# Kernel optimization log

Measured on AMD Instinct MI355X. Metric: run time of the kernel, lower is better.

The kernel has to match this reference:

```python
import jax, jax.numpy as jnp
import numpy as np

N_NODES = 100000
N_HEDGES = 25000
NNZ = 1600000
IN_CH = 128
HEADS_OUT = 128  # heads * out_channels = 8 * 16


def setup_inputs() -> dict:
    key = jax.random.key(0)
    k1, k2, k3, k4, k5, k6 = jax.random.split(key, 6)
    X = jax.random.normal(k1, (N_NODES, IN_CH), dtype=jnp.float32)
    Wlin = jax.random.normal(k2, (IN_CH, HEADS_OUT), dtype=jnp.float32) * (1.0 / np.sqrt(IN_CH))
    degE = jax.random.uniform(k3, (N_HEDGES, 1), dtype=jnp.float32)
    degV = jax.random.uniform(k4, (N_NODES, 1), dtype=jnp.float32)
    W = jnp.ones((N_HEDGES, 1), dtype=jnp.float32)
    g1_src = jax.random.randint(k5, (NNZ,), 0, N_NODES, dtype=jnp.int32)
    g1_dst = jax.random.randint(k6, (NNZ,), 0, N_HEDGES, dtype=jnp.int32)
    return {"X": X, "Wlin": Wlin, "degE": degE, "degV": degV, "W": W,
            "g1_src": g1_src, "g1_dst": g1_dst}


def reference(X, Wlin, degE, degV, W, g1_src, g1_dst):
    # Linear projection (no bias): [N, in_ch] @ [in_ch, heads*out] -> [N, HO]
    Xp = X @ Wlin
    # Stage 1: copy_u_sum over g1 (node -> hyperedge): out[e] = sum_{v in e} Xp[v]
    Xe = jax.ops.segment_sum(Xp[g1_src], g1_dst, num_segments=N_HEDGES)
    # Elementwise hyperedge scaling: degE then W (W is ones buffer in original)
    Xe = Xe * degE * W
    # Stage 2: copy_u_sum over g2 = g1^T (hyperedge -> node)
    Xv = jax.ops.segment_sum(Xe[g1_dst], g1_src, num_segments=N_NODES)
    # Node degree scaling
    Xv = Xv * degV
    return Xv
```

## Files before the change

### kernel.cpp

```cpp
#include <hip/hip_runtime.h>
#include <hip/hip_bf16.h>


#define CAPE 128
#define CAPV 64

typedef __attribute__((ext_vector_type(8))) short bf16x8;
typedef __attribute__((ext_vector_type(4))) float f32x4;
typedef __attribute__((ext_vector_type(8))) float f32x8;

__device__ __forceinline__ unsigned short f32_to_bf16(float f) {
    unsigned int u = __float_as_uint(f);
    u += 0x7FFFu + ((u >> 16) & 1u);
    return (unsigned short)(u >> 16);
}
__device__ __forceinline__ float bf16_to_f32(unsigned short h) {
    return __uint_as_float(((unsigned int)h) << 16);
}

__global__ __launch_bounds__(256) void wt_bf16(const float* __restrict__ Wl,
                                               unsigned short* __restrict__ Wt) {
    int idx = blockIdx.x * 256 + threadIdx.x;
    if (idx < 128 * 128) {
        int n = idx >> 7, k = idx & 127;
        Wt[idx] = f32_to_bf16(Wl[k * 128 + n]);
    }
}

__global__ __launch_bounds__(256) void zero_i(int* __restrict__ p, int n) {
    int i = blockIdx.x * 256 + threadIdx.x;
    if (i < n) p[i] = 0;
}

#define LDK 136
__global__ __launch_bounds__(256) void k2_fillE_gemm(const int* __restrict__ src,
                                                     const int* __restrict__ dst,
                                                     int* __restrict__ cntE,
                                                     int* __restrict__ adjE,
                                                     int nnz, int nFill,
                                                     const float* __restrict__ X,
                                                     const unsigned short* __restrict__ Wt,
                                                     unsigned short* __restrict__ Xp,
                                                     int nrows, int nGemm) {
    __shared__ unsigned short XsB[64 * LDK];
    __shared__ unsigned short WtB[128 * LDK];

    const int role = blockIdx.x & 1;
    const int id   = blockIdx.x >> 1;
    const int tid  = threadIdx.x;

    if (role == 0) {
        if (id >= nFill) return;
        const int base = id * 1024 + tid;
        int s[4], d[4], p[4];
        bool ok[4];
#pragma unroll
        for (int j = 0; j < 4; ++j) {
            int e = base + j * 256;
            ok[j] = (e < nnz);
            s[j] = ok[j] ? src[e] : 0;
            d[j] = ok[j] ? dst[e] : 0;
        }
#pragma unroll
        for (int j = 0; j < 4; ++j)
            if (ok[j]) p[j] = atomicAdd(&cntE[d[j]], 1);
#pragma unroll
        for (int j = 0; j < 4; ++j)
            if (ok[j] && p[j] < CAPE) adjE[(long)d[j] * CAPE + p[j]] = s[j];
        return;
    }

    if (id >= nGemm) return;
    const int row0 = id * 64;

    for (int base = tid * 4; base < 64 * 128; base += 1024) {
        int r = base >> 7, c = base & 127;
        float4 v = make_float4(0.f, 0.f, 0.f, 0.f);
        if (row0 + r < nrows) v = *(const float4*)(X + (long)(row0 + r) * 128 + c);
        ushort4 h;
        h.x = f32_to_bf16(v.x); h.y = f32_to_bf16(v.y);
        h.z = f32_to_bf16(v.z); h.w = f32_to_bf16(v.w);
        *(ushort4*)(XsB + r * LDK + c) = h;
    }
    for (int base = tid * 4; base < 128 * 128; base += 1024) {
        int n = base >> 7, k = base & 127;
        ushort4 h = *(const ushort4*)(Wt + base);
        *(ushort4*)(WtB + n * LDK + k) = h;
    }
    __syncthreads();

    const int w    = tid >> 6;
    const int lane = tid & 63;
    const int m    = lane & 15;
    const int quad = lane >> 4;

    f32x4 acc[8];
#pragma unroll
    for (int ct = 0; ct < 8; ++ct) acc[ct] = (f32x4){0.f, 0.f, 0.f, 0.f};

#pragma unroll
    for (int kk = 0; kk < 4; ++kk) {
        bf16x8 a = *(const bf16x8*)(XsB + (w * 16 + m) * LDK + kk * 32 + quad * 8);
#pragma unroll
        for (int ct = 0; ct < 8; ++ct) {
            bf16x8 b = *(const bf16x8*)(WtB + (ct * 16 + m) * LDK + kk * 32 + quad * 8);
            acc[ct] = __builtin_amdgcn_mfma_f32_16x16x32_bf16(a, b, acc[ct], 0, 0, 0);
        }
    }

#pragma unroll
    for (int ct = 0; ct < 8; ++ct) {
#pragma unroll
        for (int r = 0; r < 4; ++r) {
            int row = row0 + w * 16 + quad * 4 + r;
            if (row < nrows)
                Xp[(long)row * 128 + ct * 16 + m] = f32_to_bf16(acc[ct][r]);
        }
    }
}

__global__ __launch_bounds__(256) void k3_fillV_gatherE(const int* __restrict__ src,
                                                        const int* __restrict__ dst,
                                                        int* __restrict__ cntV,
                                                        unsigned short* __restrict__ adjV,
                                                        int nnz, int nFill,
                                                        const unsigned short* __restrict__ Xp,
                                                        const int* __restrict__ cntE,
                                                        const int* __restrict__ adjE,
                                                        const float* __restrict__ degE,
                                                        const float* __restrict__ Wbuf,
                                                        unsigned short* __restrict__ Xe,
                                                        int nE, int nGath) {
    const int role = blockIdx.x & 1;
    const int id   = blockIdx.x >> 1;
    const int tid  = threadIdx.x;

    if (role == 0) {
        if (id >= nFill) return;
        const int base = id * 1024 + tid;
        int s[4], d[4], p[4];
        bool ok[4];
#pragma unroll
        for (int j = 0; j < 4; ++j) {
            int e = base + j * 256;
            ok[j] = (e < nnz);
            s[j] = ok[j] ? src[e] : 0;
            d[j] = ok[j] ? dst[e] : 0;
        }
#pragma unroll
        for (int j = 0; j < 4; ++j)
            if (ok[j]) p[j] = atomicAdd(&cntV[s[j]], 1);
#pragma unroll
        for (int j = 0; j < 4; ++j)
            if (ok[j] && p[j] < CAPV) adjV[(long)s[j] * CAPV + p[j]] = (unsigned short)d[j];
        return;
    }

    if (id >= nGath) return;
    int t = id * 256 + tid;
    int e = t >> 4;
    if (e >= nE) return;
    int c = (t & 15) << 3;
    int len = cntE[e];
    if (len > CAPE) len = CAPE;
    const int* adj = adjE + (long)e * CAPE;
    float acc[8];
#pragma unroll
    for (int q = 0; q < 8; ++q) acc[q] = 0.f;

    int i = 0;
    for (; i + 8 <= len; i += 8) {
        int4 a0 = *(const int4*)(adj + i);
        int4 a1 = *(const int4*)(adj + i + 4);
        int v[8] = {a0.x, a0.y, a0.z, a0.w, a1.x, a1.y, a1.z, a1.w};
        bf16x8 h[8];
#pragma unroll
        for (int j = 0; j < 8; ++j)
            h[j] = *(const bf16x8*)(Xp + (long)v[j] * 128 + c);
#pragma unroll
        for (int j = 0; j < 8; ++j)
#pragma unroll
            for (int q = 0; q < 8; ++q)
                acc[q] += bf16_to_f32((unsigned short)h[j][q]);
    }
    for (; i + 4 <= len; i += 4) {
        int4 a0 = *(const int4*)(adj + i);
        int v[4] = {a0.x, a0.y, a0.z, a0.w};
        bf16x8 h[4];
#pragma unroll
        for (int j = 0; j < 4; ++j)
            h[j] = *(const bf16x8*)(Xp + (long)v[j] * 128 + c);
#pragma unroll
        for (int j = 0; j < 4; ++j)
#pragma unroll
            for (int q = 0; q < 8; ++q)
                acc[q] += bf16_to_f32((unsigned short)h[j][q]);
    }
    for (; i < len; ++i) {
        int v = adj[i];
        bf16x8 h = *(const bf16x8*)(Xp + (long)v * 128 + c);
#pragma unroll
        for (int q = 0; q < 8; ++q)
            acc[q] += bf16_to_f32((unsigned short)h[q]);
    }

    float sc = degE[e] * Wbuf[e];
    bf16x8 o;
#pragma unroll
    for (int q = 0; q < 8; ++q) o[q] = (short)f32_to_bf16(acc[q] * sc);
    *(bf16x8*)(Xe + (long)e * 128 + c) = o;
}

__global__ __launch_bounds__(256) void gather_nodes_b(const unsigned short* __restrict__ Xe,
                                                      const int* __restrict__ cntV,
                                                      const unsigned short* __restrict__ adjV,
                                                      const float* __restrict__ degV,
                                                      float* __restrict__ out,
                                                      int nV) {
    int t = blockIdx.x * 256 + threadIdx.x;
    int v = t >> 4;
    if (v >= nV) return;
    int c = (t & 15) << 3;
    int len = cntV[v];
    if (len > CAPV) len = CAPV;
    const unsigned short* adj = adjV + (long)v * CAPV;
    float acc[8];
#pragma unroll
    for (int q = 0; q < 8; ++q) acc[q] = 0.f;

    int i = 0;
    for (; i + 8 <= len; i += 8) {
        ushort4 a0 = *(const ushort4*)(adj + i);
        ushort4 a1 = *(const ushort4*)(adj + i + 4);
        int e[8] = {a0.x, a0.y, a0.z, a0.w, a1.x, a1.y, a1.z, a1.w};
        bf16x8 h[8];
#pragma unroll
        for (int j = 0; j < 8; ++j)
            h[j] = *(const bf16x8*)(Xe + (long)e[j] * 128 + c);
#pragma unroll
        for (int j = 0; j < 8; ++j)
#pragma unroll
            for (int q = 0; q < 8; ++q)
                acc[q] += bf16_to_f32((unsigned short)h[j][q]);
    }
    for (; i + 4 <= len; i += 4) {
        ushort4 a0 = *(const ushort4*)(adj + i);
        int e[4] = {a0.x, a0.y, a0.z, a0.w};
        bf16x8 h[4];
#pragma unroll
        for (int j = 0; j < 4; ++j)
            h[j] = *(const bf16x8*)(Xe + (long)e[j] * 128 + c);
#pragma unroll
        for (int j = 0; j < 4; ++j)
#pragma unroll
            for (int q = 0; q < 8; ++q)
                acc[q] += bf16_to_f32((unsigned short)h[j][q]);
    }
    for (; i < len; ++i) {
        int e = adj[i];
        bf16x8 h = *(const bf16x8*)(Xe + (long)e * 128 + c);
#pragma unroll
        for (int q = 0; q < 8; ++q)
            acc[q] += bf16_to_f32((unsigned short)h[q]);
    }

    float sc = degV[v];
    f32x8 o;
#pragma unroll
    for (int q = 0; q < 8; ++q) o[q] = acc[q] * sc;
    *(f32x8*)(out + (long)v * 128 + c) = o;
}

__global__ __launch_bounds__(256) void zero_f4(float4* __restrict__ p, int n4) {
    int i = blockIdx.x * 256 + threadIdx.x;
    if (i < n4) p[i] = make_float4(0.f, 0.f, 0.f, 0.f);
}

__global__ __launch_bounds__(256) void gemm_xw_f32(const float* __restrict__ X,
                                                   const float* __restrict__ Wl,
                                                   float* __restrict__ Xp,
                                                   int nrows) {
    __shared__ float Xs[32 * 128];
    const int tid = threadIdx.x;
    const int row0 = blockIdx.x * 32;
    for (int i = tid * 4; i < 32 * 128; i += 256 * 4) {
        int r = row0 + (i >> 7);
        float4 v = make_float4(0.f, 0.f, 0.f, 0.f);
        if (r < nrows) v = *(const float4*)(X + (long)row0 * 128 + i);
        *(float4*)(Xs + i) = v;
    }
    __syncthreads();
    const int col = tid & 127;
    const int rg  = (tid >> 7) * 16;
    float acc[16];
#pragma unroll
    for (int r = 0; r < 16; ++r) acc[r] = 0.f;
    for (int k = 0; k < 128; k += 4) {
        const float w0 = Wl[(k + 0) * 128 + col];
        const float w1 = Wl[(k + 1) * 128 + col];
        const float w2 = Wl[(k + 2) * 128 + col];
        const float w3 = Wl[(k + 3) * 128 + col];
#pragma unroll
        for (int r = 0; r < 16; ++r) {
            float4 x = *(const float4*)(Xs + (rg + r) * 128 + k);
            acc[r] = fmaf(x.w, w3, fmaf(x.z, w2, fmaf(x.y, w1, fmaf(x.x, w0, acc[r]))));
        }
    }
#pragma unroll
    for (int r = 0; r < 16; ++r) {
        int row = row0 + rg + r;
        if (row < nrows) Xp[(long)row * 128 + col] = acc[r];
    }
}

__global__ __launch_bounds__(256) void scatter_to_hedges(const float* __restrict__ Xp,
                                                         const int* __restrict__ src,
                                                         const int* __restrict__ dst,
                                                         float* __restrict__ Xe,
                                                         int nnz) {
    int t = blockIdx.x * 256 + threadIdx.x;
    int e = t >> 5;
    if (e >= nnz) return;
    int c = (t & 31) << 2;
    int s = src[e], d = dst[e];
    float4 v = *(const float4*)(Xp + (long)s * 128 + c);
    float* o = Xe + (long)d * 128 + c;
    atomicAdd(o + 0, v.x); atomicAdd(o + 1, v.y);
    atomicAdd(o + 2, v.z); atomicAdd(o + 3, v.w);
}

__global__ __launch_bounds__(256) void scatter_to_nodes(const float* __restrict__ Xe,
                                                        const int* __restrict__ src,
                                                        const int* __restrict__ dst,
                                                        const float* __restrict__ degE,
                                                        const float* __restrict__ Wbuf,
                                                        const float* __restrict__ degV,
                                                        float* __restrict__ out,
                                                        int nnz) {
    int t = blockIdx.x * 256 + threadIdx.x;
    int e = t >> 5;
    if (e >= nnz) return;
    int c = (t & 31) << 2;
    int s = src[e], d = dst[e];
    float sc = degE[d] * Wbuf[d] * degV[s];
    float4 v = *(const float4*)(Xe + (long)d * 128 + c);
    float* o = out + (long)s * 128 + c;
    atomicAdd(o + 0, v.x * sc); atomicAdd(o + 1, v.y * sc);
    atomicAdd(o + 2, v.z * sc); atomicAdd(o + 3, v.w * sc);
}

extern "C" void kernel_launch(void* const* d_in, const int* in_sizes, int n_in,
                              void* d_out, int out_size, void* d_ws, size_t ws_size,
                              hipStream_t stream) {
    const float* X    = (const float*)d_in[0];
    const float* Wlin = (const float*)d_in[1];
    const float* degE = (const float*)d_in[2];
    const float* degV = (const float*)d_in[3];
    const float* Wbuf = (const float*)d_in[4];
    const int* g1_src = (const int*)d_in[5];
    const int* g1_dst = (const int*)d_in[6];

    const int nE  = in_sizes[2];
    const int nV  = in_sizes[3];
    const int nnz = in_sizes[5];

    float* out = (float*)d_out;
    char* ws = (char*)d_ws;

    size_t boff = 0;
    unsigned short* Xe = (unsigned short*)(ws + boff); boff += (size_t)nE * 128 * 2;
    int* cntE   = (int*)(ws + boff);              boff += (size_t)nE * 4;
    int* cntV   = (int*)(ws + boff);              boff += (size_t)nV * 4;
    int* adjE   = (int*)(ws + boff);              boff += (size_t)nE * CAPE * 4;
    unsigned short* adjV = (unsigned short*)(ws + boff); boff += (size_t)nV * CAPV * 2;
    unsigned short* Wt   = (unsigned short*)(ws + boff); boff += (size_t)128 * 128 * 2;

    if (boff <= ws_size) {
        unsigned short* Xp_bf = (unsigned short*)d_out;

        wt_bf16<<<64, 256, 0, stream>>>(Wlin, Wt);

        int ncnt = nE + nV;
        zero_i<<<(ncnt + 255) / 256, 256, 0, stream>>>(cntE, ncnt);

        int nFill = (nnz + 1023) / 1024;
        int nGemm = (nV + 63) / 64;
        int k2max = (nFill > nGemm) ? nFill : nGemm;
        k2_fillE_gemm<<<2 * k2max, 256, 0, stream>>>(g1_src, g1_dst, cntE, adjE, nnz, nFill,
                                                     X, Wt, Xp_bf, nV, nGemm);

        int nGath = (nE * 16 + 255) / 256;
        int nGrp  = (nFill > nGath) ? nFill : nGath;
        k3_fillV_gatherE<<<2 * nGrp, 256, 0, stream>>>(g1_src, g1_dst, cntV, adjV, nnz, nFill,
                                                       Xp_bf, cntE, adjE, degE, Wbuf, Xe,
                                                       nE, nGath);

        long t = (long)nV * 16;
        gather_nodes_b<<<(int)((t + 255) / 256), 256, 0, stream>>>(Xe, cntV, adjV,
                                                                   degV, out, nV);
    } else {
        float* XeF = (float*)d_ws;
        float* Xp  = out;
        int n4 = nE * 128 / 4;
        zero_f4<<<(n4 + 255) / 256, 256, 0, stream>>>((float4*)XeF, n4);
        gemm_xw_f32<<<(nV + 31) / 32, 256, 0, stream>>>(X, Wlin, Xp, nV);
        long th = (long)nnz * 32;
        scatter_to_hedges<<<(int)((th + 255) / 256), 256, 0, stream>>>(Xp, g1_src, g1_dst,
                                                                       XeF, nnz);
        int m4 = out_size / 4;
        zero_f4<<<(m4 + 255) / 256, 256, 0, stream>>>((float4*)out, m4);
        scatter_to_nodes<<<(int)((th + 255) / 256), 256, 0, stream>>>(XeF, g1_src, g1_dst,
                                                                      degE, Wbuf, degV,
                                                                      out, nnz);
    }
}
```

Measured before the change: 335.4 us.

## Split adjacency fills and gathers into ranged chunks co-scheduled across kernels

Builds the hyperedge and node adjacency lists in key-range chunks: hyperedges in two halves, nodes in three thirds. Each fill chunk is paired in one launch with a gather over a range whose adjacency is already complete, so atomic-heavy list building overlaps bandwidth-bound gathering. The node gather no longer waits for the whole node fill to finish. The weight transpose and counter zeroing are also merged into one init kernel. In exchange, the src/dst index arrays are rescanned on every fill pass, and there are more kernel launches in total.

```diff
diff --git a/kernel.cpp b/kernel.cpp
--- a/kernel.cpp
+++ b/kernel.cpp
@@ -18,30 +18,205 @@
     return __uint_as_float(((unsigned int)h) << 16);
 }
 
-__global__ __launch_bounds__(256) void wt_bf16(const float* __restrict__ Wl,
-                                               unsigned short* __restrict__ Wt) {
-    int idx = blockIdx.x * 256 + threadIdx.x;
-    if (idx < 128 * 128) {
+
+__device__ __forceinline__ void fillE_body(const int* __restrict__ src,
+                                           const int* __restrict__ dst,
+                                           int* __restrict__ cntE,
+                                           int* __restrict__ adjE,
+                                           int nnz, int id, int tid,
+                                           int lo, int hi) {
+    const int base = id * 1024 + tid;
+    int s[4], d[4], p[4];
+    bool ok[4];
+#pragma unroll
+    for (int j = 0; j < 4; ++j) {
+        int e = base + j * 256;
+        bool in = (e < nnz);
+        s[j] = in ? src[e] : 0;
+        d[j] = in ? dst[e] : lo - 1;
+        ok[j] = in && d[j] >= lo && d[j] < hi;
+    }
+#pragma unroll
+    for (int j = 0; j < 4; ++j)
+        if (ok[j]) p[j] = atomicAdd(&cntE[d[j]], 1);
+#pragma unroll
+    for (int j = 0; j < 4; ++j)
+        if (ok[j] && p[j] < CAPE) adjE[(long)d[j] * CAPE + p[j]] = s[j];
+}
+
+__device__ __forceinline__ void fillV_body(const int* __restrict__ src,
+                                           const int* __restrict__ dst,
+                                           int* __restrict__ cntV,
+                                           unsigned short* __restrict__ adjV,
+                                           int nnz, int id, int tid,
+                                           int lo, int hi) {
+    const int base = id * 1024 + tid;
+    int s[4], d[4], p[4];
+    bool ok[4];
+#pragma unroll
+    for (int j = 0; j < 4; ++j) {
+        int e = base + j * 256;
+        bool in = (e < nnz);
+        s[j] = in ? src[e] : lo - 1;
+        d[j] = in ? dst[e] : 0;
+        ok[j] = in && s[j] >= lo && s[j] < hi;
+    }
+#pragma unroll
+    for (int j = 0; j < 4; ++j)
+        if (ok[j]) p[j] = atomicAdd(&cntV[s[j]], 1);
+#pragma unroll
+    for (int j = 0; j < 4; ++j)
+        if (ok[j] && p[j] < CAPV) adjV[(long)s[j] * CAPV + p[j]] = (unsigned short)d[j];
+}
+
+__device__ __forceinline__ void gatherE_body(int id, int tid,
+                                             const unsigned short* __restrict__ Xp,
+                                             const int* __restrict__ cntE,
+                                             const int* __restrict__ adjE,
+                                             const float* __restrict__ degE,
+                                             const float* __restrict__ Wbuf,
+                                             unsigned short* __restrict__ Xe,
+                                             int eLo, int eHi) {
+    int t = id * 256 + tid;
+    int e = eLo + (t >> 4);
+    if (e >= eHi) return;
+    int c = (t & 15) << 3;
+    int len = cntE[e];
+    if (len > CAPE) len = CAPE;
+    const int* adj = adjE + (long)e * CAPE;
+    float acc[8];
+#pragma unroll
+    for (int q = 0; q < 8; ++q) acc[q] = 0.f;
+
+    int i = 0;
+    for (; i + 8 <= len; i += 8) {
+        int4 a0 = *(const int4*)(adj + i);
+        int4 a1 = *(const int4*)(adj + i + 4);
+        int v[8] = {a0.x, a0.y, a0.z, a0.w, a1.x, a1.y, a1.z, a1.w};
+        bf16x8 h[8];
+#pragma unroll
+        for (int j = 0; j < 8; ++j)
+            h[j] = *(const bf16x8*)(Xp + (long)v[j] * 128 + c);
+#pragma unroll
+        for (int j = 0; j < 8; ++j)
+#pragma unroll
+            for (int q = 0; q < 8; ++q)
+                acc[q] += bf16_to_f32((unsigned short)h[j][q]);
+    }
+    for (; i + 4 <= len; i += 4) {
+        int4 a0 = *(const int4*)(adj + i);
+        int v[4] = {a0.x, a0.y, a0.z, a0.w};
+        bf16x8 h[4];
+#pragma unroll
+        for (int j = 0; j < 4; ++j)
+            h[j] = *(const bf16x8*)(Xp + (long)v[j] * 128 + c);
+#pragma unroll
+        for (int j = 0; j < 4; ++j)
+#pragma unroll
+            for (int q = 0; q < 8; ++q)
+                acc[q] += bf16_to_f32((unsigned short)h[j][q]);
+    }
+    for (; i < len; ++i) {
+        int v = adj[i];
+        bf16x8 h = *(const bf16x8*)(Xp + (long)v * 128 + c);
+#pragma unroll
+        for (int q = 0; q < 8; ++q)
+            acc[q] += bf16_to_f32((unsigned short)h[q]);
+    }
+
+    float sc = degE[e] * Wbuf[e];
+    bf16x8 o;
+#pragma unroll
+    for (int q = 0; q < 8; ++q) o[q] = (short)f32_to_bf16(acc[q] * sc);
+    *(bf16x8*)(Xe + (long)e * 128 + c) = o;
+}
+
+__device__ __forceinline__ void gatherV_body(int id, int tid,
+                                             const unsigned short* __restrict__ Xe,
+                                             const int* __restrict__ cntV,
+                                             const unsigned short* __restrict__ adjV,
+                                             const float* __restrict__ degV,
+                                             float* __restrict__ out,
+                                             int vLo, int vHi) {
+    int t = id * 256 + tid;
+    int v = vLo + (t >> 4);
+    if (v >= vHi) return;
+    int c = (t & 15) << 3;
+    int len = cntV[v];
+    if (len > CAPV) len = CAPV;
+    const unsigned short* adj = adjV + (long)v * CAPV;
+    float acc[8];
+#pragma unroll
+    for (int q = 0; q < 8; ++q) acc[q] = 0.f;
+
+    int i = 0;
+    for (; i + 8 <= len; i += 8) {
+        ushort4 a0 = *(const ushort4*)(adj + i);
+        ushort4 a1 = *(const ushort4*)(adj + i + 4);
+        int e[8] = {a0.x, a0.y, a0.z, a0.w, a1.x, a1.y, a1.z, a1.w};
+        bf16x8 h[8];
+#pragma unroll
+        for (int j = 0; j < 8; ++j)
+            h[j] = *(const bf16x8*)(Xe + (long)e[j] * 128 + c);
+#pragma unroll
+        for (int j = 0; j < 8; ++j)
+#pragma unroll
+            for (int q = 0; q < 8; ++q)
+                acc[q] += bf16_to_f32((unsigned short)h[j][q]);
+    }
+    for (; i + 4 <= len; i += 4) {
+        ushort4 a0 = *(const ushort4*)(adj + i);
+        int e[4] = {a0.x, a0.y, a0.z, a0.w};
+        bf16x8 h[4];
+#pragma unroll
+        for (int j = 0; j < 4; ++j)
+            h[j] = *(const bf16x8*)(Xe + (long)e[j] * 128 + c);
+#pragma unroll
+        for (int j = 0; j < 4; ++j)
+#pragma unroll
+            for (int q = 0; q < 8; ++q)
+                acc[q] += bf16_to_f32((unsigned short)h[j][q]);
+    }
+    for (; i < len; ++i) {
+        int e = adj[i];
+        bf16x8 h = *(const bf16x8*)(Xe + (long)e * 128 + c);
+#pragma unroll
+        for (int q = 0; q < 8; ++q)
+            acc[q] += bf16_to_f32((unsigned short)h[q]);
+    }
+
+    float sc = degV[v];
+    f32x8 o;
+#pragma unroll
+    for (int q = 0; q < 8; ++q) o[q] = acc[q] * sc;
+    *(f32x8*)(out + (long)v * 128 + c) = o;
+}
+
+
+__global__ __launch_bounds__(256) void k_init(const float* __restrict__ Wl,
+                                              unsigned short* __restrict__ Wt,
+                                              int* __restrict__ cnt, int ncnt) {
+    int b = blockIdx.x;
+    if (b < 64) {
+        int idx = b * 256 + threadIdx.x;
         int n = idx >> 7, k = idx & 127;
         Wt[idx] = f32_to_bf16(Wl[k * 128 + n]);
-    }
-}
-
-__global__ __launch_bounds__(256) void zero_i(int* __restrict__ p, int n) {
-    int i = blockIdx.x * 256 + threadIdx.x;
-    if (i < n) p[i] = 0;
+    } else {
+        int i = (b - 64) * 256 + threadIdx.x;
+        if (i < ncnt) cnt[i] = 0;
+    }
 }
 
 #define LDK 136
-__global__ __launch_bounds__(256) void k2_fillE_gemm(const int* __restrict__ src,
-                                                     const int* __restrict__ dst,
-                                                     int* __restrict__ cntE,
-                                                     int* __restrict__ adjE,
-                                                     int nnz, int nFill,
-                                                     const float* __restrict__ X,
-                                                     const unsigned short* __restrict__ Wt,
-                                                     unsigned short* __restrict__ Xp,
-                                                     int nrows, int nGemm) {
+__global__ __launch_bounds__(256) void k_fillE_gemm(const int* __restrict__ src,
+                                                    const int* __restrict__ dst,
+                                                    int* __restrict__ cntE,
+                                                    int* __restrict__ adjE,
+                                                    int nnz, int nFill, int eLo, int eHi,
+                                                    const float* __restrict__ X,
+                                                    const unsigned short* __restrict__ Wt,
+                                                    unsigned short* __restrict__ Xp,
+                                                    int nrows, int nGemm) {
     __shared__ unsigned short XsB[64 * LDK];
     __shared__ unsigned short WtB[128 * LDK];
 
@@ -50,23 +225,7 @@
     const int tid  = threadIdx.x;
 
     if (role == 0) {
-        if (id >= nFill) return;
-        const int base = id * 1024 + tid;
-        int s[4], d[4], p[4];
-        bool ok[4];
-#pragma unroll
-        for (int j = 0; j < 4; ++j) {
-            int e = base + j * 256;
-            ok[j] = (e < nnz);
-            s[j] = ok[j] ? src[e] : 0;
-            d[j] = ok[j] ? dst[e] : 0;
-        }
-#pragma unroll
-        for (int j = 0; j < 4; ++j)
-            if (ok[j]) p[j] = atomicAdd(&cntE[d[j]], 1);
-#pragma unroll
-        for (int j = 0; j < 4; ++j)
-            if (ok[j] && p[j] < CAPE) adjE[(long)d[j] * CAPE + p[j]] = s[j];
+        if (id < nFill) fillE_body(src, dst, cntE, adjE, nnz, id, tid, eLo, eHi);
         return;
     }
 
@@ -119,156 +278,74 @@
     }
 }
 
-__global__ __launch_bounds__(256) void k3_fillV_gatherE(const int* __restrict__ src,
-                                                        const int* __restrict__ dst,
-                                                        int* __restrict__ cntV,
-                                                        unsigned short* __restrict__ adjV,
-                                                        int nnz, int nFill,
-                                                        const unsigned short* __restrict__ Xp,
-                                                        const int* __restrict__ cntE,
-                                                        const int* __restrict__ adjE,
-                                                        const float* __restrict__ degE,
-                                                        const float* __restrict__ Wbuf,
-                                                        unsigned short* __restrict__ Xe,
-                                                        int nE, int nGath) {
+__global__ __launch_bounds__(256) void k_fillE_gatherE(const int* __restrict__ src,
+                                                       const int* __restrict__ dst,
+                                                       int* __restrict__ cntE,
+                                                       int* __restrict__ adjE,
+                                                       int nnz, int nFill, int eLo, int eHi,
+                                                       const unsigned short* __restrict__ Xp,
+                                                       const float* __restrict__ degE,
+                                                       const float* __restrict__ Wbuf,
+                                                       unsigned short* __restrict__ Xe,
+                                                       int geLo, int geHi) {
     const int role = blockIdx.x & 1;
     const int id   = blockIdx.x >> 1;
     const int tid  = threadIdx.x;
-
     if (role == 0) {
-        if (id >= nFill) return;
-        const int base = id * 1024 + tid;
-        int s[4], d[4], p[4];
-        bool ok[4];
-#pragma unroll
-        for (int j = 0; j < 4; ++j) {
-            int e = base + j * 256;
-            ok[j] = (e < nnz);
-            s[j] = ok[j] ? src[e] : 0;
-            d[j] = ok[j] ? dst[e] : 0;
-        }
-#pragma unroll
-        for (int j = 0; j < 4; ++j)
-            if (ok[j]) p[j] = atomicAdd(&cntV[s[j]], 1);
-#pragma unroll
-        for (int j = 0; j < 4; ++j)
-            if (ok[j] && p[j] < CAPV) adjV[(long)s[j] * CAPV + p[j]] = (unsigned short)d[j];
-        return;
-    }
-
-    if (id >= nGath) return;
-    int t = id * 256 + tid;
-    int e = t >> 4;
-    if (e >= nE) return;
-    int c = (t & 15) << 3;
-    int len = cntE[e];
-    if (len > CAPE) len = CAPE;
-    const int* adj = adjE + (long)e * CAPE;
-    float acc[8];
-#pragma unroll
-    for (int q = 0; q < 8; ++q) acc[q] = 0.f;
-
-    int i = 0;
-    for (; i + 8 <= len; i += 8) {
-        int4 a0 = *(const int4*)(adj + i);
-        int4 a1 = *(const int4*)(adj + i + 4);
-        int v[8] = {a0.x, a0.y, a0.z, a0.w, a1.x, a1.y, a1.z, a1.w};
-        bf16x8 h[8];
-#pragma unroll
-        for (int j = 0; j < 8; ++j)
-            h[j] = *(const bf16x8*)(Xp + (long)v[j] * 128 + c);
-#pragma unroll
-        for (int j = 0; j < 8; ++j)
-#pragma unroll
-            for (int q = 0; q < 8; ++q)
-                acc[q] += bf16_to_f32((unsigned short)h[j][q]);
-    }
-    for (; i + 4 <= len; i += 4) {
-        int4 a0 = *(const int4*)(adj + i);
-        int v[4] = {a0.x, a0.y, a0.z, a0.w};
-        bf16x8 h[4];
-#pragma unroll
-        for (int j = 0; j < 4; ++j)
-            h[j] = *(const bf16x8*)(Xp + (long)v[j] * 128 + c);
-#pragma unroll
-        for (int j = 0; j < 4; ++j)
-#pragma unroll
-            for (int q = 0; q < 8; ++q)
-                acc[q] += bf16_to_f32((unsigned short)h[j][q]);
-    }
-    for (; i < len; ++i) {
-        int v = adj[i];
-        bf16x8 h = *(const bf16x8*)(Xp + (long)v * 128 + c);
-#pragma unroll
-        for (int q = 0; q < 8; ++q)
-            acc[q] += bf16_to_f32((unsigned short)h[q]);
-    }
-
-    float sc = degE[e] * Wbuf[e];
-    bf16x8 o;
-#pragma unroll
-    for (int q = 0; q < 8; ++q) o[q] = (short)f32_to_bf16(acc[q] * sc);
-    *(bf16x8*)(Xe + (long)e * 128 + c) = o;
-}
-
-__global__ __launch_bounds__(256) void gather_nodes_b(const unsigned short* __restrict__ Xe,
-                                                      const int* __restrict__ cntV,
-                                                      const unsigned short* __restrict__ adjV,
-                                                      const float* __restrict__ degV,
-                                                      float* __restrict__ out,
-                                                      int nV) {
-    int t = blockIdx.x * 256 + threadIdx.x;
-    int v = t >> 4;
-    if (v >= nV) return;
-    int c = (t & 15) << 3;
-    int len = cntV[v];
-    if (len > CAPV) len = CAPV;
-    const unsigned short* adj = adjV + (long)v * CAPV;
-    float acc[8];
-#pragma unroll
-    for (int q = 0; q < 8; ++q) acc[q] = 0.f;
-
-    int i = 0;
-    for (; i + 8 <= len; i += 8) {
-        ushort4 a0 = *(const ushort4*)(adj + i);
-        ushort4 a1 = *(const ushort4*)(adj + i + 4);
-        int e[8] = {a0.x, a0.y, a0.z, a0.w, a1.x, a1.y, a1.z, a1.w};
-        bf16x8 h[8];
-#pragma unroll
-        for (int j = 0; j < 8; ++j)
-            h[j] = *(const bf16x8*)(Xe + (long)e[j] * 128 + c);
-#pragma unroll
-        for (int j = 0; j < 8; ++j)
-#pragma unroll
-            for (int q = 0; q < 8; ++q)
-                acc[q] += bf16_to_f32((unsigned short)h[j][q]);
-    }
-    for (; i + 4 <= len; i += 4) {
-        ushort4 a0 = *(const ushort4*)(adj + i);
-        int e[4] = {a0.x, a0.y, a0.z, a0.w};
-        bf16x8 h[4];
-#pragma unroll
-        for (int j = 0; j < 4; ++j)
-            h[j] = *(const bf16x8*)(Xe + (long)e[j] * 128 + c);
-#pragma unroll
-        for (int j = 0; j < 4; ++j)
-#pragma unroll
-            for (int q = 0; q < 8; ++q)
-                acc[q] += bf16_to_f32((unsigned short)h[j][q]);
-    }
-    for (; i < len; ++i) {
-        int e = adj[i];
-        bf16x8 h = *(const bf16x8*)(Xe + (long)e * 128 + c);
-#pragma unroll
-        for (int q = 0; q < 8; ++q)
-            acc[q] += bf16_to_f32((unsigned short)h[q]);
-    }
-
-    float sc = degV[v];
-    f32x8 o;
-#pragma unroll
-    for (int q = 0; q < 8; ++q) o[q] = acc[q] * sc;
-    *(f32x8*)(out + (long)v * 128 + c) = o;
+        if (id < nFill) fillE_body(src, dst, cntE, adjE, nnz, id, tid, eLo, eHi);
+    } else {
+        gatherE_body(id, tid, Xp, cntE, adjE, degE, Wbuf, Xe, geLo, geHi);
+    }
+}
+
+__global__ __launch_bounds__(256) void k_fillV_gatherE(const int* __restrict__ src,
+                                                       const int* __restrict__ dst,
+                                                       int* __restrict__ cntV,
+                                                       unsigned short* __restrict__ adjV,
+                                                       int nnz, int nFill, int vLo, int vHi,
+                                                       const unsigned short* __restrict__ Xp,
+                                                       const int* __restrict__ cntE,
+                                                       const int* __restrict__ adjE,
+                                                       const float* __restrict__ degE,
+                                                       const float* __restrict__ Wbuf,
+                                                       unsigned short* __restrict__ Xe,
+                                                       int geLo, int geHi) {
+    const int role = blockIdx.x & 1;
+    const int id   = blockIdx.x >> 1;
+    const int tid  = threadIdx.x;
+    if (role == 0) {
+        if (id < nFill) fillV_body(src, dst, cntV, adjV, nnz, id, tid, vLo, vHi);
+    } else {
+        gatherE_body(id, tid, Xp, cntE, adjE, degE, Wbuf, Xe, geLo, geHi);
+    }
+}
+
+__global__ __launch_bounds__(256) void k_fillV_gatherV(const int* __restrict__ src,
+                                                       const int* __restrict__ dst,
+                                                       int* __restrict__ cntV,
+                                                       unsigned short* __restrict__ adjV,
+                                                       int nnz, int nFill, int vLo, int vHi,
+                                                       const unsigned short* __restrict__ Xe,
+                                                       const float* __restrict__ degV,
+                                                       float* __restrict__ out,
+                                                       int gvLo, int gvHi) {
+    const int role = blockIdx.x & 1;
+    const int id   = blockIdx.x >> 1;
+    const int tid  = threadIdx.x;
+    if (role == 0) {
+        if (id < nFill) fillV_body(src, dst, cntV, adjV, nnz, id, tid, vLo, vHi);
+    } else {
+        gatherV_body(id, tid, Xe, cntV, adjV, degV, out, gvLo, gvHi);
+    }
+}
+
+__global__ __launch_bounds__(256) void k_gatherV(const unsigned short* __restrict__ Xe,
+                                                 const int* __restrict__ cntV,
+                                                 const unsigned short* __restrict__ adjV,
+                                                 const float* __restrict__ degV,
+                                                 float* __restrict__ out,
+                                                 int gvLo, int gvHi) {
+    gatherV_body(blockIdx.x, threadIdx.x, Xe, cntV, adjV, degV, out, gvLo, gvHi);
 }
 
 __global__ __launch_bounds__(256) void zero_f4(float4* __restrict__ p, int n4) {
@@ -378,26 +455,43 @@
     if (boff <= ws_size) {
         unsigned short* Xp_bf = (unsigned short*)d_out;
 
-        wt_bf16<<<64, 256, 0, stream>>>(Wlin, Wt);
+        const int nFill = (nnz + 1023) / 1024;
+        const int nGemm = (nV + 63) / 64;
+        const int eMid  = nE / 2;
+        const int v1 = (nV / 3) & ~15;
+        const int v2 = ((2 * nV) / 3) & ~15;
 
         int ncnt = nE + nV;
-        zero_i<<<(ncnt + 255) / 256, 256, 0, stream>>>(cntE, ncnt);
-
-        int nFill = (nnz + 1023) / 1024;
-        int nGemm = (nV + 63) / 64;
-        int k2max = (nFill > nGemm) ? nFill : nGemm;
-        k2_fillE_gemm<<<2 * k2max, 256, 0, stream>>>(g1_src, g1_dst, cntE, adjE, nnz, nFill,
-                                                     X, Wt, Xp_bf, nV, nGemm);
-
-        int nGath = (nE * 16 + 255) / 256;
-        int nGrp  = (nFill > nGath) ? nFill : nGath;
-        k3_fillV_gatherE<<<2 * nGrp, 256, 0, stream>>>(g1_src, g1_dst, cntV, adjV, nnz, nFill,
-                                                       Xp_bf, cntE, adjE, degE, Wbuf, Xe,
-                                                       nE, nGath);
-
-        long t = (long)nV * 16;
-        gather_nodes_b<<<(int)((t + 255) / 256), 256, 0, stream>>>(Xe, cntV, adjV,
-                                                                   degV, out, nV);
+        k_init<<<64 + (ncnt + 255) / 256, 256, 0, stream>>>(Wlin, Wt, cntE, ncnt);
+
+        int g2a = 2 * ((nFill > nGemm) ? nFill : nGemm);
+        k_fillE_gemm<<<g2a, 256, 0, stream>>>(g1_src, g1_dst, cntE, adjE, nnz, nFill,
+                                              0, eMid, X, Wt, Xp_bf, nV, nGemm);
+
+        int nGE1 = (eMid * 16 + 255) / 256;
+        int g2b = 2 * ((nFill > nGE1) ? nFill : nGE1);
+        k_fillE_gatherE<<<g2b, 256, 0, stream>>>(g1_src, g1_dst, cntE, adjE, nnz, nFill,
+                                                 eMid, nE, Xp_bf, degE, Wbuf, Xe,
+                                                 0, eMid);
+
+        int nGE2 = ((nE - eMid) * 16 + 255) / 256;
+        int g3 = 2 * ((nFill > nGE2) ? nFill : nGE2);
+        k_fillV_gatherE<<<g3, 256, 0, stream>>>(g1_src, g1_dst, cntV, adjV, nnz, nFill,
+                                                0, v1, Xp_bf, cntE, adjE, degE, Wbuf, Xe,
+                                                eMid, nE);
+
+        int nGV1 = (v1 * 16 + 255) / 256;
+        int g4 = 2 * ((nFill > nGV1) ? nFill : nGV1);
+        k_fillV_gatherV<<<g4, 256, 0, stream>>>(g1_src, g1_dst, cntV, adjV, nnz, nFill,
+                                                v1, v2, Xe, degV, out, 0, v1);
+
+        int nGV2 = ((v2 - v1) * 16 + 255) / 256;
+        int g5 = 2 * ((nFill > nGV2) ? nFill : nGV2);
+        k_fillV_gatherV<<<g5, 256, 0, stream>>>(g1_src, g1_dst, cntV, adjV, nnz, nFill,
+                                                v2, nV, Xe, degV, out, v1, v2);
+
+        int nGV3 = ((nV - v2) * 16 + 255) / 256;
+        k_gatherV<<<nGV3, 256, 0, stream>>>(Xe, cntV, adjV, degV, out, v2, nV);
     } else {
         float* XeF = (float*)d_ws;
         float* Xp  = out;
```

Result: slower. 357.0 us (+6.4%).

## Build adjacency lists with chunked LDS histograms and scan instead of global atomics

Applied to the files above, without the earlier changes.

Replaces the global-atomic bucket fill of both adjacency lists with a three-pass build. Each block histograms one chunk of edges into packed 8-bit counters held in shared memory, a scan kernel turns these into per-chunk offsets, and a scatter pass writes the slots using shared-memory atomics. The GEMM and fill roles are split back into separate kernels, and the histV and Xe buffers share one region. The aim is to remove contention from global atomics. The cost is extra passes over src/dst, a byte-per-chunk histogram that can overflow when a chunk holds more than 255 edges for one key, and a serial per-column scan.

```diff
diff --git a/kernel.cpp b/kernel.cpp
--- a/kernel.cpp
+++ b/kernel.cpp
@@ -4,6 +4,8 @@
 
 #define CAPE 128
 #define CAPV 64
+#define LDK  136
+#define RW   6250
 
 typedef __attribute__((ext_vector_type(8))) short bf16x8;
 typedef __attribute__((ext_vector_type(4))) float f32x4;
@@ -18,8 +20,8 @@
     return __uint_as_float(((unsigned int)h) << 16);
 }
 
-__global__ __launch_bounds__(256) void wt_bf16(const float* __restrict__ Wl,
-                                               unsigned short* __restrict__ Wt) {
+__global__ __launch_bounds__(256) void k_init(const float* __restrict__ Wl,
+                                              unsigned short* __restrict__ Wt) {
     int idx = blockIdx.x * 256 + threadIdx.x;
     if (idx < 128 * 128) {
         int n = idx >> 7, k = idx & 127;
@@ -27,50 +29,14 @@
     }
 }
 
-__global__ __launch_bounds__(256) void zero_i(int* __restrict__ p, int n) {
-    int i = blockIdx.x * 256 + threadIdx.x;
-    if (i < n) p[i] = 0;
-}
-
-#define LDK 136
-__global__ __launch_bounds__(256) void k2_fillE_gemm(const int* __restrict__ src,
-                                                     const int* __restrict__ dst,
-                                                     int* __restrict__ cntE,
-                                                     int* __restrict__ adjE,
-                                                     int nnz, int nFill,
-                                                     const float* __restrict__ X,
-                                                     const unsigned short* __restrict__ Wt,
-                                                     unsigned short* __restrict__ Xp,
-                                                     int nrows, int nGemm) {
+__global__ __launch_bounds__(256) void k_gemm(const float* __restrict__ X,
+                                              const unsigned short* __restrict__ Wt,
+                                              unsigned short* __restrict__ Xp,
+                                              int nrows) {
     __shared__ unsigned short XsB[64 * LDK];
     __shared__ unsigned short WtB[128 * LDK];
-
-    const int role = blockIdx.x & 1;
-    const int id   = blockIdx.x >> 1;
-    const int tid  = threadIdx.x;
-
-    if (role == 0) {
-        if (id >= nFill) return;
-        const int base = id * 1024 + tid;
-        int s[4], d[4], p[4];
-        bool ok[4];
-#pragma unroll
-        for (int j = 0; j < 4; ++j) {
-            int e = base + j * 256;
-            ok[j] = (e < nnz);
-            s[j] = ok[j] ? src[e] : 0;
-            d[j] = ok[j] ? dst[e] : 0;
-        }
-#pragma unroll
-        for (int j = 0; j < 4; ++j)
-            if (ok[j]) p[j] = atomicAdd(&cntE[d[j]], 1);
-#pragma unroll
-        for (int j = 0; j < 4; ++j)
-            if (ok[j] && p[j] < CAPE) adjE[(long)d[j] * CAPE + p[j]] = s[j];
-        return;
-    }
-
-    if (id >= nGemm) return;
+    const int id  = blockIdx.x;
+    const int tid = threadIdx.x;
     const int row0 = id * 64;
 
     for (int base = tid * 4; base < 64 * 128; base += 1024) {
@@ -107,7 +73,6 @@
             acc[ct] = __builtin_amdgcn_mfma_f32_16x16x32_bf16(a, b, acc[ct], 0, 0, 0);
         }
     }
-
 #pragma unroll
     for (int ct = 0; ct < 8; ++ct) {
 #pragma unroll
@@ -119,45 +84,122 @@
     }
 }
 
-__global__ __launch_bounds__(256) void k3_fillV_gatherE(const int* __restrict__ src,
-                                                        const int* __restrict__ dst,
-                                                        int* __restrict__ cntV,
-                                                        unsigned short* __restrict__ adjV,
-                                                        int nnz, int nFill,
-                                                        const unsigned short* __restrict__ Xp,
-                                                        const int* __restrict__ cntE,
-                                                        const int* __restrict__ adjE,
-                                                        const float* __restrict__ degE,
-                                                        const float* __restrict__ Wbuf,
-                                                        unsigned short* __restrict__ Xe,
-                                                        int nE, int nGath) {
-    const int role = blockIdx.x & 1;
-    const int id   = blockIdx.x >> 1;
-    const int tid  = threadIdx.x;
-
-    if (role == 0) {
-        if (id >= nFill) return;
-        const int base = id * 1024 + tid;
-        int s[4], d[4], p[4];
-        bool ok[4];
-#pragma unroll
-        for (int j = 0; j < 4; ++j) {
-            int e = base + j * 256;
-            ok[j] = (e < nnz);
-            s[j] = ok[j] ? src[e] : 0;
-            d[j] = ok[j] ? dst[e] : 0;
-        }
-#pragma unroll
-        for (int j = 0; j < 4; ++j)
-            if (ok[j]) p[j] = atomicAdd(&cntV[s[j]], 1);
-#pragma unroll
-        for (int j = 0; j < 4; ++j)
-            if (ok[j] && p[j] < CAPV) adjV[(long)s[j] * CAPV + p[j]] = (unsigned short)d[j];
-        return;
-    }
-
-    if (id >= nGath) return;
-    int t = id * 256 + tid;
+__global__ __launch_bounds__(256) void k_hist(const int* __restrict__ keyE,
+                                              const int* __restrict__ keyV,
+                                              int nnz,
+                                              unsigned int* __restrict__ histE32,
+                                              unsigned int* __restrict__ histV32,
+                                              int nE4, int nV4, int che, int chv,
+                                              int nchE, int nrE, int nchV, int nrV) {
+    __shared__ unsigned int s32[RW];
+    int bid = blockIdx.x;
+    const int tid = threadIdx.x;
+    const int* key; unsigned int* hist; int n4, ch, c, r;
+    if (bid < nchE * nrE) {
+        key = keyE; hist = histE32; n4 = nE4; ch = che;
+        c = bid % nchE; r = bid / nchE;
+    } else {
+        bid -= nchE * nrE;
+        key = keyV; hist = histV32; n4 = nV4; ch = chv;
+        c = bid % nchV; r = bid / nchV;
+    }
+    const int w0 = r * RW;
+    const int w1 = (w0 + RW < n4) ? (w0 + RW) : n4;
+    const int nw = w1 - w0;
+    for (int i = tid; i < nw; i += 256) s32[i] = 0;
+    __syncthreads();
+    int e0 = c * ch, e1 = e0 + ch; if (e1 > nnz) e1 = nnz;
+    for (int e = e0 + tid; e < e1; e += 256) {
+        int k = key[e];
+        int w = k >> 2;
+        if (w >= w0 && w < w1)
+            atomicAdd(&s32[w - w0], 1u << ((k & 3) * 8));
+    }
+    __syncthreads();
+    for (int i = tid; i < nw; i += 256)
+        hist[(long)c * n4 + w0 + i] = s32[i];
+}
+
+__global__ __launch_bounds__(256) void k_scan(unsigned char* __restrict__ histE8,
+                                              unsigned char* __restrict__ histV8,
+                                              int* __restrict__ cntE,
+                                              int* __restrict__ cntV,
+                                              int nE, int nV, int nchE, int nchV) {
+    int t = blockIdx.x * 256 + threadIdx.x;
+    if (t < nE) {
+        int b = t, run = 0;
+        for (int c = 0; c < nchE; ++c) {
+            long a = (long)c * nE + b;
+            int h = histE8[a];
+            histE8[a] = (unsigned char)run;
+            run += h;
+        }
+        cntE[b] = run;
+    } else if (t < nE + nV) {
+        int v = t - nE, run = 0;
+        for (int c = 0; c < nchV; ++c) {
+            long a = (long)c * nV + v;
+            int h = histV8[a];
+            histV8[a] = (unsigned char)run;
+            run += h;
+        }
+        cntV[v] = run;
+    }
+}
+
+__global__ __launch_bounds__(256) void k_scatter(const int* __restrict__ src,
+                                                 const int* __restrict__ dst,
+                                                 int nnz,
+                                                 const unsigned char* __restrict__ histE8,
+                                                 const unsigned char* __restrict__ histV8,
+                                                 int* __restrict__ adjE,
+                                                 unsigned short* __restrict__ adjV,
+                                                 int nE4, int nV4, int che, int chv,
+                                                 int nchE, int nrE, int nchV, int nrV) {
+    __shared__ unsigned int c32[RW];
+    __shared__ unsigned int sbase[RW];
+    int bid = blockIdx.x;
+    const int tid = threadIdx.x;
+    const bool isE = bid < nchE * nrE;
+    const int* key; const int* val; const unsigned int* hist; int n4, ch, c, r;
+    if (isE) {
+        key = dst; val = src; hist = (const unsigned int*)histE8; n4 = nE4; ch = che;
+        c = bid % nchE; r = bid / nchE;
+    } else {
+        bid -= nchE * nrE;
+        key = src; val = dst; hist = (const unsigned int*)histV8; n4 = nV4; ch = chv;
+        c = bid % nchV; r = bid / nchV;
+    }
+    const int w0 = r * RW;
+    const int w1 = (w0 + RW < n4) ? (w0 + RW) : n4;
+    const int nw = w1 - w0;
+    const unsigned int* brow = hist + (long)c * n4 + w0;
+    for (int i = tid; i < nw; i += 256) { c32[i] = 0; sbase[i] = brow[i]; }
+    __syncthreads();
+    int e0 = c * ch, e1 = e0 + ch; if (e1 > nnz) e1 = nnz;
+    for (int e = e0 + tid; e < e1; e += 256) {
+        int k = key[e];
+        int w = k >> 2;
+        if (w < w0 || w >= w1) continue;
+        int sh = (k & 3) * 8;
+        unsigned int old = atomicAdd(&c32[w - w0], 1u << sh);
+        int slot = (int)((sbase[w - w0] >> sh) & 0xFF) + (int)((old >> sh) & 0xFF);
+        if (isE) {
+            if (slot < CAPE) adjE[(long)k * CAPE + slot] = val[e];
+        } else {
+            if (slot < CAPV) adjV[(long)k * CAPV + slot] = (unsigned short)val[e];
+        }
+    }
+}
+
+__global__ __launch_bounds__(256) void k_gatherE(const unsigned short* __restrict__ Xp,
+                                                 const int* __restrict__ cntE,
+                                                 const int* __restrict__ adjE,
+                                                 const float* __restrict__ degE,
+                                                 const float* __restrict__ Wbuf,
+                                                 unsigned short* __restrict__ Xe,
+                                                 int nE) {
+    int t = blockIdx.x * 256 + threadIdx.x;
     int e = t >> 4;
     if (e >= nE) return;
     int c = (t & 15) << 3;
@@ -211,12 +253,12 @@
     *(bf16x8*)(Xe + (long)e * 128 + c) = o;
 }
 
-__global__ __launch_bounds__(256) void gather_nodes_b(const unsigned short* __restrict__ Xe,
-                                                      const int* __restrict__ cntV,
-                                                      const unsigned short* __restrict__ adjV,
-                                                      const float* __restrict__ degV,
-                                                      float* __restrict__ out,
-                                                      int nV) {
+__global__ __launch_bounds__(256) void k_gatherV(const unsigned short* __restrict__ Xe,
+                                                 const int* __restrict__ cntV,
+                                                 const unsigned short* __restrict__ adjV,
+                                                 const float* __restrict__ degV,
+                                                 float* __restrict__ out,
+                                                 int nV) {
     int t = blockIdx.x * 256 + threadIdx.x;
     int v = t >> 4;
     if (v >= nV) return;
@@ -367,37 +409,75 @@
     float* out = (float*)d_out;
     char* ws = (char*)d_ws;
 
-    size_t boff = 0;
-    unsigned short* Xe = (unsigned short*)(ws + boff); boff += (size_t)nE * 128 * 2;
-    int* cntE   = (int*)(ws + boff);              boff += (size_t)nE * 4;
-    int* cntV   = (int*)(ws + boff);              boff += (size_t)nV * 4;
-    int* adjE   = (int*)(ws + boff);              boff += (size_t)nE * CAPE * 4;
-    unsigned short* adjV = (unsigned short*)(ws + boff); boff += (size_t)nV * CAPV * 2;
-    unsigned short* Wt   = (unsigned short*)(ws + boff); boff += (size_t)128 * 128 * 2;
-
-    if (boff <= ws_size) {
+    auto layout_size = [&](int cE, int cV) -> size_t {
+        size_t o = 0;
+        o += (size_t)nE * CAPE * 4;
+        o += (size_t)nV * CAPV * 2;
+        o += (size_t)nE * 4 + (size_t)nV * 4;
+        o += (size_t)cE * nE;
+        size_t hv = (size_t)cV * nV;
+        size_t xe = (size_t)nE * 128 * 2;
+        o += (hv > xe) ? hv : xe;
+        o += 128 * 128 * 2;
+        o += 4096;
+        return o;
+    };
+
+    int nchE = 64, nchV = 64;
+    if (layout_size(nchE, nchV) > ws_size) { nchE = 32; nchV = 32; }
+
+    const bool aligned4 = ((nE & 3) == 0) && ((nV & 3) == 0);
+
+    if (aligned4 && layout_size(nchE, nchV) <= ws_size) {
+        size_t boff = 0;
+        auto alloc = [&](size_t bytes) -> char* {
+            char* p = ws + boff;
+            boff += (bytes + 255) & ~(size_t)255;
+            return p;
+        };
+        int* adjE            = (int*)alloc((size_t)nE * CAPE * 4);
+        unsigned short* adjV = (unsigned short*)alloc((size_t)nV * CAPV * 2);
+        int* cntE            = (int*)alloc((size_t)nE * 4);
+        int* cntV            = (int*)alloc((size_t)nV * 4);
+        unsigned char* histE8 = (unsigned char*)alloc((size_t)nchE * nE);
+        size_t hv = (size_t)nchV * nV;
+        size_t xe = (size_t)nE * 128 * 2;
+        char* region          = alloc((hv > xe) ? hv : xe);
+        unsigned char* histV8 = (unsigned char*)region;
+        unsigned short* Xe    = (unsigned short*)region;
+        unsigned short* Wt    = (unsigned short*)alloc((size_t)128 * 128 * 2);
+
         unsigned short* Xp_bf = (unsigned short*)d_out;
 
-        wt_bf16<<<64, 256, 0, stream>>>(Wlin, Wt);
-
-        int ncnt = nE + nV;
-        zero_i<<<(ncnt + 255) / 256, 256, 0, stream>>>(cntE, ncnt);
-
-        int nFill = (nnz + 1023) / 1024;
+        const int nE4 = nE >> 2, nV4 = nV >> 2;
+        const int nrE = (nE4 + RW - 1) / RW;
+        const int nrV = (nV4 + RW - 1) / RW;
+        const int che = (nnz + nchE - 1) / nchE;
+        const int chv = (nnz + nchV - 1) / nchV;
+
+        k_init<<<64, 256, 0, stream>>>(Wlin, Wt);
+
         int nGemm = (nV + 63) / 64;
-        int k2max = (nFill > nGemm) ? nFill : nGemm;
-        k2_fillE_gemm<<<2 * k2max, 256, 0, stream>>>(g1_src, g1_dst, cntE, adjE, nnz, nFill,
-                                                     X, Wt, Xp_bf, nV, nGemm);
-
-        int nGath = (nE * 16 + 255) / 256;
-        int nGrp  = (nFill > nGath) ? nFill : nGath;
-        k3_fillV_gatherE<<<2 * nGrp, 256, 0, stream>>>(g1_src, g1_dst, cntV, adjV, nnz, nFill,
-                                                       Xp_bf, cntE, adjE, degE, Wbuf, Xe,
-                                                       nE, nGath);
-
-        long t = (long)nV * 16;
-        gather_nodes_b<<<(int)((t + 255) / 256), 256, 0, stream>>>(Xe, cntV, adjV,
-                                                                   degV, out, nV);
+        k_gemm<<<nGemm, 256, 0, stream>>>(X, Wt, Xp_bf, nV);
+
+        k_hist<<<nchE * nrE + nchV * nrV, 256, 0, stream>>>(
+            g1_dst, g1_src, nnz,
+            (unsigned int*)histE8, (unsigned int*)histV8,
+            nE4, nV4, che, chv, nchE, nrE, nchV, nrV);
+
+        k_scan<<<(nE + nV + 255) / 256, 256, 0, stream>>>(histE8, histV8,
+                                                          cntE, cntV,
+                                                          nE, nV, nchE, nchV);
+
+        k_scatter<<<nchE * nrE + nchV * nrV, 256, 0, stream>>>(
+            g1_src, g1_dst, nnz, histE8, histV8, adjE, adjV,
+            nE4, nV4, che, chv, nchE, nrE, nchV, nrV);
+
+        int gE = (nE * 16 + 255) / 256;
+        k_gatherE<<<gE, 256, 0, stream>>>(Xp_bf, cntE, adjE, degE, Wbuf, Xe, nE);
+
+        int gV = (nV * 16 + 255) / 256;
+        k_gatherV<<<gV, 256, 0, stream>>>(Xe, cntV, adjV, degV, out, nV);
     } else {
         float* XeF = (float*)d_ws;
         float* Xp  = out;
```

New measurement: 382.1 us. 13.9% more time.
